# Kernel optimization log

Hardware: AMD Instinct MI355X
Metric: run time of the kernel (lower is better)

## Reference

```python
import jax, jax.numpy as jnp
import numpy as np

B = 128          # episodes
L = 512          # static pad length per episode (support or query)
LAMBDA_K_TAU = 0.1


def _masked_cov(x, mask, lengths):
    # x: [B, L, D]; mask: [B, L, 1]; lengths: [B] (float counts)
    x = x * mask
    mean = x.sum(axis=1) / lengths[:, None]                    # [B, D]
    c = (x - mean[:, None, :]) * mask                          # [B, L, D]
    cov = jnp.einsum('bld,ble->bde', c, c)                     # [B, D, D]
    return cov / (lengths - 1.0)[:, None, None]


def _calc_label_cov_inv(task_cov, label_cov):
    d = task_cov.shape[-1]
    eye = jnp.eye(d, dtype=task_cov.dtype)
    m = LAMBDA_K_TAU * label_cov + (1.0 - LAMBDA_K_TAU) * task_cov + 0.1 * eye
    return jnp.linalg.inv(m)


def _separate_qsl(graph_reprs, labels, is_query, batch_index):
    # Re-batch flat [N, D] into padded per-episode support/query tensors.
    N, D = graph_reprs.shape
    g = batch_index * 2 + is_query                             # group id
    perm = jnp.argsort(g)                                      # stable sort
    gs = g[perm]
    first = jnp.searchsorted(gs, gs, side='left')
    rank = jnp.arange(N) - first                               # index within group
    b = batch_index[perm]
    q = is_query[perm]
    row_s = jnp.where(q == 0, rank, L)                         # dummy row L for other kind
    row_q = jnp.where(q == 1, rank, L)
    xp = graph_reprs[perm]
    sup = jnp.zeros((B, L + 1, D), graph_reprs.dtype).at[b, row_s].set(xp)[:, :L]
    qry = jnp.zeros((B, L + 1, D), graph_reprs.dtype).at[b, row_q].set(xp)[:, :L]
    sup_lab = jnp.zeros((B, L + 1), labels.dtype).at[b, row_s].set(labels[perm])[:, :L]
    isq = is_query.astype(jnp.float32)
    sup_len = jnp.zeros((B,), jnp.float32).at[batch_index].add(1.0 - isq)
    qry_len = jnp.zeros((B,), jnp.float32).at[batch_index].add(isq)
    return sup, sup_lab, sup_len, qry, qry_len


def setup_inputs() -> dict:
    key = jax.random.key(0)
    k0, k1, k2, k3 = jax.random.split(key, 4)
    N, D = 49152, 512
    graph_reprs = jax.random.normal(k0, (N, D), jnp.float32)
    labels = jax.random.randint(k1, (N,), 0, 2)
    is_query = jax.random.randint(k2, (N,), 0, 2)
    batch_index = jnp.sort(jax.random.randint(k3, (N,), 0, B))
    log_scale = jnp.full((1,), np.log(1.0 / 16.0), jnp.float32)
    return {"graph_reprs": graph_reprs, "log_scale": log_scale,
            "labels": labels, "is_query": is_query, "batch_index": batch_index}


def reference(graph_reprs, log_scale, labels, is_query, batch_index):
    sup, sup_lab, sup_len, qry, qry_len = _separate_qsl(graph_reprs, labels, is_query, batch_index)
    f = jnp.float32
    support_mask = (jnp.arange(L)[None, :] < sup_len[:, None]).astype(f)[..., None]  # [B,L,1]
    mpos = (sup_lab == 1).astype(f)[..., None] * support_mask
    mneg = (sup_lab == 0).astype(f)[..., None] * support_mask

    pos_mean = (sup * mpos).sum(axis=1) / mpos.sum(axis=1)     # [B, D]
    neg_mean = (sup * mneg).sum(axis=1) / mneg.sum(axis=1)

    task_cov = _masked_cov(sup, support_mask, sup_len)
    pos_cnt = mpos.sum(axis=(1, 2))
    neg_cnt = mneg.sum(axis=(1, 2))
    # Masked covariance == cov of boolean-extracted, re-batched class subsets.
    pos_cov = _masked_cov(sup, mpos, pos_cnt)
    neg_cov = _masked_cov(sup, mneg, neg_cnt)

    pos_inv = _calc_label_cov_inv(task_cov, pos_cov)
    neg_inv = _calc_label_cov_inv(task_cov, neg_cov)

    query_mask = (jnp.arange(L)[None, :] < qry_len[:, None]).astype(f)  # [B, L]
    pos_diff = qry - pos_mean[:, None, :]
    neg_diff = qry - neg_mean[:, None, :]
    # Faithful to original einsum (sums inv over its second index):
    pos_maha = jnp.einsum('bik,bkx,bij->bi', pos_diff, pos_inv, pos_diff) * query_mask
    neg_maha = jnp.einsum('bik,bkx,bij->bi', neg_diff, neg_inv, neg_diff) * query_mask

    logits = jnp.stack([neg_maha, pos_maha], axis=-1)          # [B, L, 2]
    return logits * jnp.exp(log_scale)
```

## Files before the change

kernel.cpp:

```cpp
#include <hip/hip_runtime.h>
#include <cstdint>
#include <cstddef>

#define EPISODES 128
#define LPAD     512
#define DDIM     512
#define NS_CAP   320
#define GTILE    64
#define NPAIRS   15
#define CG_ITERS 14
#define GL_F4    4096
#define KCH      64
#define XBF_ROW  1024
#define GREG     48

typedef __attribute__((ext_vector_type(8))) __bf16 bf16x8;
typedef __attribute__((ext_vector_type(4))) float  floatx4;

__device__ __forceinline__ int lower_bound_dev(const int* __restrict__ a, int n, int key){
    int lo = 0, hi = n;
    while(lo < hi){
        int m = (lo + hi) >> 1;
        if(a[m] < key) lo = m + 1; else hi = m;
    }
    return lo;
}

__device__ __forceinline__ float4 f4add(float4 a, float4 b){
    return make_float4(a.x+b.x, a.y+b.y, a.z+b.z, a.w+b.w);
}
__device__ __forceinline__ float4 f4fma(float s, float4 a, float4 acc){
    return make_float4(acc.x + s*a.x, acc.y + s*a.y, acc.z + s*a.z, acc.w + s*a.w);
}
__device__ __forceinline__ float f4dot(float4 a, float4 b){
    return a.x*b.x + a.y*b.y + a.z*b.z + a.w*b.w;
}
__device__ __forceinline__ float f4sum(float4 a){ return (a.x+a.y)+(a.z+a.w); }

__device__ __forceinline__ unsigned short f2bf(float x){
    unsigned u = __float_as_uint(x);
    u += 0x7FFFu + ((u >> 16) & 1u);
    return (unsigned short)(u >> 16);
}
__device__ __forceinline__ float bf2f(unsigned short h){
    return __uint_as_float(((unsigned)h) << 16);
}
__device__ __forceinline__ void cvt_hilo(float4 x, ushort4& hh, ushort4& ll){
    hh.x = f2bf(x.x); ll.x = f2bf(x.x - bf2f(hh.x));
    hh.y = f2bf(x.y); ll.y = f2bf(x.y - bf2f(hh.y));
    hh.z = f2bf(x.z); ll.z = f2bf(x.z - bf2f(hh.z));
    hh.w = f2bf(x.w); ll.w = f2bf(x.w - bf2f(hh.w));
}

__device__ __forceinline__ float rdlanef(float v, int l){
    return __int_as_float(__builtin_amdgcn_readlane(__float_as_int(v), l));
}
__device__ __forceinline__ float dotb(float4 g, float4 u, int l){
    return g.x*rdlanef(u.x,l) + g.y*rdlanef(u.y,l)
         + g.z*rdlanef(u.z,l) + g.w*rdlanef(u.w,l);
}
__device__ __forceinline__ void gload_lds16(const void* g, void* l){
    __builtin_amdgcn_global_load_lds(
        (const __attribute__((address_space(1))) void*)g,
        (__attribute__((address_space(3))) void*)l,
        16, 0, 0);
}

__global__ __launch_bounds__(256) void k_prep(
        const int* __restrict__ labels, const int* __restrict__ is_query,
        const int* __restrict__ bidx, const float* __restrict__ X, int N,
        int* __restrict__ sup_idx, int* __restrict__ qry_idx,
        int* __restrict__ sup_lab, int* __restrict__ counts,
        float* __restrict__ task_mean, float* __restrict__ pos_mean,
        float* __restrict__ neg_mean, float* __restrict__ row_sums2,
        unsigned short* __restrict__ Xbf)
{
    const int bid  = blockIdx.x;
    const int b    = bid >> 1;
    const int h    = bid & 1;
    const int tid  = threadIdx.x;
    const int lane = tid & 63;
    const int wave = tid >> 6;

    __shared__ int s_start, s_end;
    __shared__ int wq[4];
    __shared__ int s_runq, s_npos;
    __shared__ int   sidx[NS_CAP];
    __shared__ float slabf[NS_CAP];
    __shared__ float4 pa[4][64];
    __shared__ float4 pp[4][64];

    if(tid == 0){
        s_start = lower_bound_dev(bidx, N, b);
        s_end   = lower_bound_dev(bidx, N, b + 1);
        s_runq  = 0;
        s_npos  = 0;
    }
    __syncthreads();
    const int start = s_start, end = s_end;

    for(int base = start; base < end; base += 256){
        int idx   = base + tid;
        bool valid = idx < end;
        int q   = valid ? is_query[idx] : 0;
        int lab = valid ? labels[idx]   : 0;
        unsigned long long m = __ballot(q == 1);
        if(lane == 0) wq[wave] = __popcll(m);
        __syncthreads();
        int woff = 0;
        for(int w = 0; w < wave; w++) woff += wq[w];
        int qbefore = __popcll(m & ((1ull << lane) - 1ull)) + woff;
        int runq0 = s_runq;
        int chunk_total = wq[0] + wq[1] + wq[2] + wq[3];
        if(valid){
            int pos_in_seg = idx - start;
            if(q){
                int qr = runq0 + qbefore;
                if(h == 0 && qr < LPAD) qry_idx[b * LPAD + qr] = idx;
            } else {
                int sr = pos_in_seg - runq0 - qbefore;
                if(sr < LPAD){
                    if(h == 0){
                        sup_idx[b * LPAD + sr] = idx;
                        sup_lab[b * LPAD + sr] = lab;
                    }
                    if(sr < NS_CAP){ sidx[sr] = idx; slabf[sr] = (float)lab; }
                    if(lab == 1) atomicAdd(&s_npos, 1);
                }
            }
        }
        __syncthreads();
        if(tid == 0) s_runq = runq0 + chunk_total;
        __syncthreads();
    }

    const int nq   = s_runq;
    const int ns   = (end - start) - nq;
    const int npos = s_npos;
    const int nneg = ns - npos;
    if(h == 0 && tid == 0){
        counts[b*4 + 0] = ns;
        counts[b*4 + 1] = nq;
        counts[b*4 + 2] = npos;
        counts[b*4 + 3] = nneg;
    }
    const int nsb = min(ns, NS_CAP);

    const float4* X4 = (const float4*)X;
    const int colg = h*64 + lane;
    float4 sa = make_float4(0.f,0.f,0.f,0.f);
    float4 sp = make_float4(0.f,0.f,0.f,0.f);
    int r = wave;
    for(; r + 12 < nsb; r += 16){
        int n0 = sidx[r], n1 = sidx[r+4], n2 = sidx[r+8], n3 = sidx[r+12];
        float l0 = slabf[r], l1 = slabf[r+4], l2 = slabf[r+8], l3 = slabf[r+12];
        float4 x0 = X4[(size_t)n0*128 + colg];
        float4 x1 = X4[(size_t)n1*128 + colg];
        float4 x2 = X4[(size_t)n2*128 + colg];
        float4 x3 = X4[(size_t)n3*128 + colg];
        sa = f4add(sa, f4add(f4add(x0,x1), f4add(x2,x3)));
        sp = f4fma(l0,x0, f4fma(l1,x1, f4fma(l2,x2, f4fma(l3,x3, sp))));
        {
            ushort4 hh, ll;
            size_t rb;
            rb = ((size_t)(b*NS_CAP + r   ) << 10);
            cvt_hilo(x0, hh, ll);
            *(ushort4*)&Xbf[rb + colg*4] = hh;  *(ushort4*)&Xbf[rb + 512 + colg*4] = ll;
            rb = ((size_t)(b*NS_CAP + r+4 ) << 10);
            cvt_hilo(x1, hh, ll);
            *(ushort4*)&Xbf[rb + colg*4] = hh;  *(ushort4*)&Xbf[rb + 512 + colg*4] = ll;
            rb = ((size_t)(b*NS_CAP + r+8 ) << 10);
            cvt_hilo(x2, hh, ll);
            *(ushort4*)&Xbf[rb + colg*4] = hh;  *(ushort4*)&Xbf[rb + 512 + colg*4] = ll;
            rb = ((size_t)(b*NS_CAP + r+12) << 10);
            cvt_hilo(x3, hh, ll);
            *(ushort4*)&Xbf[rb + colg*4] = hh;  *(ushort4*)&Xbf[rb + 512 + colg*4] = ll;
        }
        float r0s = f4sum(x0), r1s = f4sum(x1), r2s = f4sum(x2), r3s = f4sum(x3);
        #pragma unroll
        for(int off = 32; off; off >>= 1){
            r0s += __shfl_xor(r0s, off); r1s += __shfl_xor(r1s, off);
            r2s += __shfl_xor(r2s, off); r3s += __shfl_xor(r3s, off);
        }
        if(lane == 0){
            row_sums2[(b*LPAD + r   )*2 + h] = r0s;
            row_sums2[(b*LPAD + r+4 )*2 + h] = r1s;
            row_sums2[(b*LPAD + r+8 )*2 + h] = r2s;
            row_sums2[(b*LPAD + r+12)*2 + h] = r3s;
        }
    }
    for(; r < nsb; r += 4){
        int n = sidx[r];
        float l = slabf[r];
        float4 x = X4[(size_t)n*128 + colg];
        sa = f4add(sa, x);
        sp = f4fma(l, x, sp);
        {
            ushort4 hh, ll;
            size_t rb = ((size_t)(b*NS_CAP + r) << 10);
            cvt_hilo(x, hh, ll);
            *(ushort4*)&Xbf[rb + colg*4] = hh;  *(ushort4*)&Xbf[rb + 512 + colg*4] = ll;
        }
        float rs = f4sum(x);
        #pragma unroll
        for(int off = 32; off; off >>= 1) rs += __shfl_xor(rs, off);
        if(lane == 0) row_sums2[(b*LPAD + r)*2 + h] = rs;
    }
    {
        const int padf = min((nsb + 63) & ~63, NS_CAP);
        ushort4 z; z.x = z.y = z.z = z.w = 0;
        for(int rz = nsb + wave; rz < padf; rz += 4){
            size_t rb = ((size_t)(b*NS_CAP + rz) << 10);
            *(ushort4*)&Xbf[rb + colg*4] = z;
            *(ushort4*)&Xbf[rb + 512 + colg*4] = z;
        }
    }
    pa[wave][lane] = sa;
    pp[wave][lane] = sp;
    __syncthreads();
    if(tid < 64){
        float4 A = f4add(f4add(pa[0][tid],pa[1][tid]), f4add(pa[2][tid],pa[3][tid]));
        float4 P = f4add(f4add(pp[0][tid],pp[1][tid]), f4add(pp[2][tid],pp[3][tid]));
        float4 Nn = make_float4(A.x-P.x, A.y-P.y, A.z-P.z, A.w-P.w);
        float ia = 1.f/(float)ns, ip = 1.f/(float)npos, in = 1.f/(float)nneg;
        int c = b*128 + h*64 + tid;
        ((float4*)task_mean)[c] = make_float4(A.x*ia, A.y*ia, A.z*ia, A.w*ia);
        ((float4*)pos_mean )[c] = make_float4(P.x*ip, P.y*ip, P.z*ip, P.w*ip);
        ((float4*)neg_mean )[c] = make_float4(Nn.x*in, Nn.y*in, Nn.z*in, Nn.w*in);
    }
}

__global__ __launch_bounds__(256) void k_gram(
        const unsigned short* __restrict__ Xbf,
        const int* __restrict__ counts, float* __restrict__ G0)
{
    const int bid = blockIdx.x;
    const int b   = bid / NPAIRS;
    int tp = bid % NPAIRS;
    int ti = 0;
    while((ti+1)*(ti+2)/2 <= tp) ti++;
    const int tj  = tp - ti*(ti+1)/2;
    const int tid = threadIdx.x;
    const int lane = tid & 63;
    const int wave = tid >> 6;

    const int ns  = counts[b*4 + 0];
    const int nsc = min(ns, NS_CAP);
    if(ti * GTILE >= nsc) return;
    const bool diag = (ti == tj);

    __shared__ __align__(16) unsigned short SM[4 * GTILE * 64];
    unsigned short* const SAh = SM;
    unsigned short* const SAl = SM + 4096;
    const unsigned short* Bh = diag ? SAh : (SM + 8192);
    const unsigned short* Bl = diag ? SAl : (SM + 12288);

    const int r8  = lane >> 3;
    const int blk = lane & 7;
    const int fr = lane & 15;
    const int fq = (lane >> 4) * 8;
    const int ry = (wave >> 1) * 32;
    const int cx = (wave & 1) * 32;

    floatx4 acc[2][2];
    acc[0][0] = (floatx4){0.f,0.f,0.f,0.f};
    acc[0][1] = (floatx4){0.f,0.f,0.f,0.f};
    acc[1][0] = (floatx4){0.f,0.f,0.f,0.f};
    acc[1][1] = (floatx4){0.f,0.f,0.f,0.f};

    const int xr = blk ^ r8;
    for(int k0 = 0; k0 < DDIM; k0 += KCH){
        __syncthreads();
        #pragma unroll
        for(int i = 0; i < 4; i++){
            int e  = wave*4 + i;
            int pl = e >> 3, g = e & 7;
            int row = g*8 + r8;
            const unsigned short* src = Xbf
                + ((size_t)(b*NS_CAP + ti*GTILE + row) << 10)
                + pl*512 + k0 + (xr << 3);
            gload_lds16(src, SM + pl*4096 + row*64 + blk*8);
        }
        if(!diag){
            #pragma unroll
            for(int i = 0; i < 4; i++){
                int e  = wave*4 + i;
                int pl = e >> 3, g = e & 7;
                int row = g*8 + r8;
                const unsigned short* src = Xbf
                    + ((size_t)(b*NS_CAP + tj*GTILE + row) << 10)
                    + pl*512 + k0 + (xr << 3);
                gload_lds16(src, SM + 8192 + pl*4096 + row*64 + blk*8);
            }
        }
        __syncthreads();
        #pragma unroll
        for(int ks = 0; ks < KCH; ks += 32){
            const int j  = (ks + fq) >> 3;
            const int jx = (j ^ (fr & 7)) << 3;
            bf16x8 ah0 = *(const bf16x8*)&SAh[(ry      + fr)*64 + jx];
            bf16x8 ah1 = *(const bf16x8*)&SAh[(ry + 16 + fr)*64 + jx];
            bf16x8 al0 = *(const bf16x8*)&SAl[(ry      + fr)*64 + jx];
            bf16x8 al1 = *(const bf16x8*)&SAl[(ry + 16 + fr)*64 + jx];
            bf16x8 bh0 = *(const bf16x8*)&Bh [(cx      + fr)*64 + jx];
            bf16x8 bh1 = *(const bf16x8*)&Bh [(cx + 16 + fr)*64 + jx];
            bf16x8 bl0 = *(const bf16x8*)&Bl [(cx      + fr)*64 + jx];
            bf16x8 bl1 = *(const bf16x8*)&Bl [(cx + 16 + fr)*64 + jx];
            acc[0][0] = __builtin_amdgcn_mfma_f32_16x16x32_bf16(ah0, bh0, acc[0][0], 0,0,0);
            acc[0][1] = __builtin_amdgcn_mfma_f32_16x16x32_bf16(ah0, bh1, acc[0][1], 0,0,0);
            acc[1][0] = __builtin_amdgcn_mfma_f32_16x16x32_bf16(ah1, bh0, acc[1][0], 0,0,0);
            acc[1][1] = __builtin_amdgcn_mfma_f32_16x16x32_bf16(ah1, bh1, acc[1][1], 0,0,0);
            acc[0][0] = __builtin_amdgcn_mfma_f32_16x16x32_bf16(ah0, bl0, acc[0][0], 0,0,0);
            acc[0][1] = __builtin_amdgcn_mfma_f32_16x16x32_bf16(ah0, bl1, acc[0][1], 0,0,0);
            acc[1][0] = __builtin_amdgcn_mfma_f32_16x16x32_bf16(ah1, bl0, acc[1][0], 0,0,0);
            acc[1][1] = __builtin_amdgcn_mfma_f32_16x16x32_bf16(ah1, bl1, acc[1][1], 0,0,0);
            acc[0][0] = __builtin_amdgcn_mfma_f32_16x16x32_bf16(al0, bh0, acc[0][0], 0,0,0);
            acc[0][1] = __builtin_amdgcn_mfma_f32_16x16x32_bf16(al0, bh1, acc[0][1], 0,0,0);
            acc[1][0] = __builtin_amdgcn_mfma_f32_16x16x32_bf16(al1, bh0, acc[1][0], 0,0,0);
            acc[1][1] = __builtin_amdgcn_mfma_f32_16x16x32_bf16(al1, bh1, acc[1][1], 0,0,0);
        }
    }

    float4* Gf4 = (float4*)(G0 + (size_t)b * NS_CAP * NS_CAP);
    const int q = lane >> 4, j = lane & 15;
    #pragma unroll
    for(int sy = 0; sy < 2; sy++)
        #pragma unroll
        for(int sx = 0; sx < 2; sx++){
            int cq = ((ti*GTILE + ry + sy*16) >> 2) + q;
            int t  = tj*GTILE + cx + sx*16 + j;
            Gf4[(size_t)cq * NS_CAP + t] =
                make_float4(acc[sy][sx].x, acc[sy][sx].y, acc[sy][sx].z, acc[sy][sx].w);
        }

    if(!diag){
        __syncthreads();
        float* Tb = (float*)SM;
        #pragma unroll
        for(int sy = 0; sy < 2; sy++)
            #pragma unroll
            for(int sx = 0; sx < 2; sx++){
                int r0 = ry + sy*16 + 4*q;
                int c  = cx + sx*16 + j;
                Tb[(r0+0)*68 + c] = acc[sy][sx].x;
                Tb[(r0+1)*68 + c] = acc[sy][sx].y;
                Tb[(r0+2)*68 + c] = acc[sy][sx].z;
                Tb[(r0+3)*68 + c] = acc[sy][sx].w;
            }
        __syncthreads();
        for(int e = tid; e < 16*GTILE; e += 256){
            int cc = e >> 6;
            int r  = e & 63;
            float4 v = *(const float4*)&Tb[r*68 + 4*cc];
            Gf4[(size_t)(tj*16 + cc) * NS_CAP + ti*GTILE + r] = v;
        }
    }
}

extern __shared__ float4 gl4[];

__global__ __launch_bounds__(512) void k_cgc(
        const float* __restrict__ X, const float* __restrict__ G0,
        const int* __restrict__ sup_idx, const int* __restrict__ sup_lab,
        const int* __restrict__ counts, const float* __restrict__ row_sums2,
        float* __restrict__ vout)
{
    const int bid  = blockIdx.x;
    const int sys  = ((bid & 7) << 5) | (bid >> 3);
    const int b    = sys >> 1;
    const int cls  = sys & 1;
    const int tid  = threadIdx.x;
    const int lane = tid & 63;
    const int wave = tid >> 6;

    __shared__ __align__(16) float u[NS_CAP];
    __shared__ int   idx_l[NS_CAP];
    __shared__ float P[64];

    const int ns   = counts[b*4 + 0];
    const int nsc  = min(ns, NS_CAP);
    const int ncls = cls ? counts[b*4 + 2] : counts[b*4 + 3];
    const float c_task = 0.9f / (float)(ns - 1);
    const float c_cls  = 0.1f / (float)(ncls - 1);
    const float inv_ns = 1.f / (float)ns;
    const float inv_nc = 1.f / (float)ncls;
    const float4* G4 = (const float4*)(G0 + (size_t)b * NS_CAP * NS_CAP);
    const float4* u4 = (const float4*)u;
    const int nf4 = (nsc + 3) >> 2;

    const bool mth = tid < NS_CAP;
    const bool own = tid < nsc;
    float mfl = 0.f, sraw = 0.f;
    if(own){
        mfl  = (sup_lab[b*LPAD + tid] == cls) ? 1.f : 0.f;
        float2 rs = ((const float2*)row_sums2)[b*LPAD + tid];
        sraw = rs.x + rs.y;
    }
    for(int s = tid; s < nsc; s += 512) idx_l[s] = sup_idx[b*LPAD + s];
    if(tid < 64) P[tid] = 0.f;

    const bool fastu   = (nf4 <= 64);
    const bool haverow = ((wave << 6) < nsc);

    float4 g[GREG];
    if(fastu && haverow){
        #pragma unroll
        for(int c4 = 0; c4 < GREG; c4++){
            float4 v = G4[(size_t)c4 * NS_CAP + tid];
            bool live = (4*c4 < nsc);
            g[c4].x = live ? v.x : 0.f;
            g[c4].y = live ? v.y : 0.f;
            g[c4].z = live ? v.z : 0.f;
            g[c4].w = live ? v.w : 0.f;
        }
    }

    if(fastu && nf4 > GREG){
        const int nchunk = (nsc + 63) >> 6;
        for(int ch = 0; ch < nchunk; ch++){
            const int t = (ch << 6) + lane;
            const bool act = t < nsc;
            for(int c4 = GREG + wave; c4 < nf4; c4 += 8){
                if(act) gload_lds16(G4 + (size_t)c4 * NS_CAP + t,
                                    gl4 + (c4 - GREG) * nsc + t);
            }
        }
    }
    __syncthreads();

    auto bundle = [&](float v0, float v1, float v2, float v3, float v4,
                      float* S){
        #pragma unroll
        for(int off = 32; off; off >>= 1){
            v0 += __shfl_xor(v0, off); v1 += __shfl_xor(v1, off);
            v2 += __shfl_xor(v2, off); v3 += __shfl_xor(v3, off);
            v4 += __shfl_xor(v4, off);
        }
        if(lane == 0){
            P[wave*8 + 0] = v0; P[wave*8 + 1] = v1; P[wave*8 + 2] = v2;
            P[wave*8 + 3] = v3; P[wave*8 + 4] = v4;
        }
        __syncthreads();
        float pv = P[lane];
        pv += __shfl_xor(pv, 8);
        pv += __shfl_xor(pv, 16);
        pv += __shfl_xor(pv, 32);
        S[0] = __shfl(pv, 0); S[1] = __shfl(pv, 1); S[2] = __shfl(pv, 2);
        S[3] = __shfl(pv, 3); S[4] = __shfl(pv, 4);
    };

    auto matvec = [&]() -> float {
        float t = 0.f;
        if(fastu){
            if(haverow){
                float4 ubc = u4[lane < nf4 ? lane : 0];
                asm volatile("" : "+v"(ubc.x), "+v"(ubc.y), "+v"(ubc.z), "+v"(ubc.w));
                float s0 = 0.f, s1 = 0.f, s2 = 0.f, s3 = 0.f;
                #pragma unroll
                for(int c4 = 0; c4 < GREG; c4 += 4){
                    s0 += dotb(g[c4+0], ubc, c4+0);
                    s1 += dotb(g[c4+1], ubc, c4+1);
                    s2 += dotb(g[c4+2], ubc, c4+2);
                    s3 += dotb(g[c4+3], ubc, c4+3);
                }
                if(nf4 > GREG){
                    const int row = own ? tid : (nsc - 1);
                    for(int c4 = GREG; c4 < nf4; c4++)
                        s0 += f4dot(gl4[(c4 - GREG)*nsc + row], u4[c4]);
                }
                t = (s0 + s1) + (s2 + s3);
            }
            return own ? t : 0.f;
        } else {
            float s0 = 0.f, s1 = 0.f, s2 = 0.f, s3 = 0.f;
            if(own){
                int c4 = 0;
                for(; c4 + 4 <= nf4; c4 += 4){
                    float4 h0 = G4[(size_t)(c4+0)*NS_CAP + tid];
                    float4 h1 = G4[(size_t)(c4+1)*NS_CAP + tid];
                    float4 h2 = G4[(size_t)(c4+2)*NS_CAP + tid];
                    float4 h3 = G4[(size_t)(c4+3)*NS_CAP + tid];
                    s0 += f4dot(h0, u4[c4+0]); s1 += f4dot(h1, u4[c4+1]);
                    s2 += f4dot(h2, u4[c4+2]); s3 += f4dot(h3, u4[c4+3]);
                }
                for(; c4 < nf4; c4++) s0 += f4dot(G4[(size_t)c4*NS_CAP + tid], u4[c4]);
            }
            float tt = (s0 + s1) + (s2 + s3);
            return own ? tt : 0.f;
        }
    };

    float S[5];
    bundle(sraw, mfl * sraw, 0.f, 0.f, 0.f, S);
    float A0 = S[0] * inv_ns, A1 = S[1] * inv_nc;
    float cr = own ? -10.f * (c_task*(sraw - A0) + mfl*c_cls*(sraw - A1)) : 0.f;
    if(mth) u[tid] = cr;
    __syncthreads();
    float tr = matvec();

    float cp = 0.f, cq = 0.f, tq = 0.f, cx = 0.f;
    float gamma_old = 1.f, alpha_old = 1.f;
    bool first = true;

    for(int it = 0; it < CG_ITERS; ++it){
        bundle(tr, mfl*tr, tr*tr, mfl*tr*tr, tr*cr, S);
        A0 = S[0] * inv_ns; A1 = S[1] * inv_nc;
        float gamma = S[4];
        float delta = 0.1f*gamma + c_task*(S[2] - S[0]*A0)
                                 + c_cls *(S[3] - S[1]*A1);
        float beta  = first ? 0.f : gamma / gamma_old;
        float denom = first ? delta : (delta - beta * gamma / alpha_old);
        float alpha = (gamma < 1e-30f) ? 0.f : gamma / denom;
        float ur = own ? (c_task*(tr - A0) + mfl*c_cls*(tr - A1)) : 0.f;
        float cw = 0.1f*cr + ur;
        cp = cr + beta * cp;
        cq = cw + beta * cq;
        cx += alpha * cp;
        if(it == CG_ITERS - 1 || gamma < 1e-26f) break;
        if(mth) u[tid] = ur;
        __syncthreads();
        float gv = matvec();
        float tw = 0.1f*tr + gv;
        tq = tw + beta * tq;
        cr -= alpha * cq;
        tr -= alpha * tq;
        gamma_old = gamma; alpha_old = alpha; first = false;
    }

    __syncthreads();
    if(mth) u[tid] = own ? cx : 0.f;
    __syncthreads();
    const float4* X4 = (const float4*)X;
    const int f4c = tid & 127;
    const int rg  = tid >> 7;
    float4 acc = make_float4(0.f,0.f,0.f,0.f);
    int s = rg;
    for(; s + 28 < nsc; s += 32){
        int n0 = idx_l[s],    n1 = idx_l[s+4],  n2 = idx_l[s+8],  n3 = idx_l[s+12];
        int n4 = idx_l[s+16], n5 = idx_l[s+20], n6 = idx_l[s+24], n7 = idx_l[s+28];
        float w0 = u[s],    w1 = u[s+4],  w2 = u[s+8],  w3 = u[s+12];
        float w4 = u[s+16], w5 = u[s+20], w6 = u[s+24], w7 = u[s+28];
        float4 x0 = X4[(size_t)n0*128 + f4c];
        float4 x1 = X4[(size_t)n1*128 + f4c];
        float4 x2 = X4[(size_t)n2*128 + f4c];
        float4 x3 = X4[(size_t)n3*128 + f4c];
        float4 x4 = X4[(size_t)n4*128 + f4c];
        float4 x5 = X4[(size_t)n5*128 + f4c];
        float4 x6 = X4[(size_t)n6*128 + f4c];
        float4 x7 = X4[(size_t)n7*128 + f4c];
        acc = f4fma(w0,x0, f4fma(w1,x1, f4fma(w2,x2, f4fma(w3,x3, acc))));
        acc = f4fma(w4,x4, f4fma(w5,x5, f4fma(w6,x6, f4fma(w7,x7, acc))));
    }
    for(; s < nsc; s += 4)
        acc = f4fma(u[s], X4[(size_t)idx_l[s]*128 + f4c], acc);
    gl4[rg*128 + f4c] = acc;
    __syncthreads();
    if(tid < 128){
        float4 v = f4add(f4add(gl4[tid], gl4[128+tid]),
                         f4add(gl4[256+tid], gl4[384+tid]));
        v.x += 10.f; v.y += 10.f; v.z += 10.f; v.w += 10.f;
        ((float4*)vout)[(size_t)sys * 128 + tid] = v;
    }
}

__global__ __launch_bounds__(256) void k_out(
        const float* __restrict__ X,
        const int* __restrict__ qry_idx, const int* __restrict__ counts,
        const float* __restrict__ pos_mean, const float* __restrict__ neg_mean,
        const float* __restrict__ vsol, const float* __restrict__ log_scale,
        float* __restrict__ out)
{
    const int bid  = blockIdx.x;
    const int b    = bid >> 1;
    const int h    = bid & 1;
    const int tid  = threadIdx.x;
    const int lane = tid & 63;
    const int wave = tid >> 6;

    __shared__ __align__(16) float vpos[DDIM];
    __shared__ __align__(16) float vneg[DDIM];
    __shared__ float red4[4][4];
    __shared__ float sc[4];

    const int nq  = counts[b*4 + 1];
    const int nqc = min(nq, LPAD);
    const float scale = expf(log_scale[0]);

    float pm0 = pos_mean[b*DDIM + tid], pm1 = pos_mean[b*DDIM + tid + 256];
    float nm0 = neg_mean[b*DDIM + tid], nm1 = neg_mean[b*DDIM + tid + 256];
    float vp0 = vsol[(size_t)(b*2 + 1) * DDIM + tid];
    float vp1 = vsol[(size_t)(b*2 + 1) * DDIM + tid + 256];
    float vn0 = vsol[(size_t)(b*2 + 0) * DDIM + tid];
    float vn1 = vsol[(size_t)(b*2 + 0) * DDIM + tid + 256];
    vpos[tid] = vp0; vpos[tid + 256] = vp1;
    vneg[tid] = vn0; vneg[tid + 256] = vn1;

    float smp = pm0 + pm1;
    float smn = nm0 + nm1;
    float mvp = pm0 * vp0 + pm1 * vp1;
    float mvn = nm0 * vn0 + nm1 * vn1;
    #pragma unroll
    for(int off = 32; off; off >>= 1){
        smp += __shfl_xor(smp, off);
        smn += __shfl_xor(smn, off);
        mvp += __shfl_xor(mvp, off);
        mvn += __shfl_xor(mvn, off);
    }
    if(lane == 0){
        red4[wave][0] = smp; red4[wave][1] = smn;
        red4[wave][2] = mvp; red4[wave][3] = mvn;
    }
    __syncthreads();
    if(tid < 4) sc[tid] = red4[0][tid] + red4[1][tid] + red4[2][tid] + red4[3][tid];
    __syncthreads();

    const float4* vp4 = (const float4*)vpos;
    const float4* vn4 = (const float4*)vneg;
    const float4 vpa = vp4[lane], vpb = vp4[lane + 64];
    const float4 vna = vn4[lane], vnb = vn4[lane + 64];
    for(int r = wave + 4*h; r < nqc; r += 16){
        int r2 = r + 8;
        bool has2 = r2 < nqc;
        int n  = qry_idx[b * LPAD + r];
        int n2 = qry_idx[b * LPAD + (has2 ? r2 : r)];
        const float4* xr = (const float4*)(X + (size_t)n  * DDIM);
        const float4* yr = (const float4*)(X + (size_t)n2 * DDIM);
        float4 x0 = xr[lane], x1 = xr[lane + 64];
        float4 y0 = yr[lane], y1 = yr[lane + 64];
        float tp = f4dot(x0, vpa) + f4dot(x1, vpb);
        float tn = f4dot(x0, vna) + f4dot(x1, vnb);
        float sx = f4sum(x0) + f4sum(x1);
        float tp2 = f4dot(y0, vpa) + f4dot(y1, vpb);
        float tn2 = f4dot(y0, vna) + f4dot(y1, vnb);
        float sx2 = f4sum(y0) + f4sum(y1);
        #pragma unroll
        for(int off = 32; off; off >>= 1){
            tp  += __shfl_xor(tp,  off);
            tn  += __shfl_xor(tn,  off);
            sx  += __shfl_xor(sx,  off);
            tp2 += __shfl_xor(tp2, off);
            tn2 += __shfl_xor(tn2, off);
            sx2 += __shfl_xor(sx2, off);
        }
        if(lane == 0){
            float mp = (tp - sc[2]) * (sx - sc[0]);
            float mn = (tn - sc[3]) * (sx - sc[1]);
            ((float2*)out)[(size_t)b * LPAD + r] = make_float2(mn * scale, mp * scale);
            if(has2){
                float mp2 = (tp2 - sc[2]) * (sx2 - sc[0]);
                float mn2 = (tn2 - sc[3]) * (sx2 - sc[1]);
                ((float2*)out)[(size_t)b * LPAD + r2] = make_float2(mn2 * scale, mp2 * scale);
            }
        }
    }
    const int lo = max(nqc, h * 256), hi = (h + 1) * 256;
    for(int r = lo + tid; r < hi; r += 256)
        ((float2*)out)[(size_t)b * LPAD + r] = make_float2(0.f, 0.f);
}

extern "C" void kernel_launch(void* const* d_in, const int* in_sizes, int n_in,
                              void* d_out, int out_size, void* d_ws, size_t ws_size,
                              hipStream_t stream)
{
    const float* X         = (const float*)d_in[0];
    const float* log_scale = (const float*)d_in[1];
    const int*   labels    = (const int*)d_in[2];
    const int*   is_query  = (const int*)d_in[3];
    const int*   bidx      = (const int*)d_in[4];
    const int N = in_sizes[2];

    char* ws = (char*)d_ws;
    auto alloc = [&](size_t bytes) -> char* {
        char* p = ws;
        ws += (bytes + 255) & ~(size_t)255;
        return p;
    };
    int*   sup_idx   = (int*)  alloc((size_t)EPISODES * LPAD * sizeof(int));
    int*   qry_idx   = (int*)  alloc((size_t)EPISODES * LPAD * sizeof(int));
    int*   sup_lab   = (int*)  alloc((size_t)EPISODES * LPAD * sizeof(int));
    int*   counts    = (int*)  alloc((size_t)EPISODES * 4 * sizeof(int));
    float* task_mean = (float*)alloc((size_t)EPISODES * DDIM * sizeof(float));
    float* pos_mean  = (float*)alloc((size_t)EPISODES * DDIM * sizeof(float));
    float* neg_mean  = (float*)alloc((size_t)EPISODES * DDIM * sizeof(float));
    float* vsol      = (float*)alloc((size_t)EPISODES * 2 * DDIM * sizeof(float));
    float* row_sums2 = (float*)alloc((size_t)EPISODES * LPAD * 2 * sizeof(float));
    float* G0        = (float*)alloc((size_t)EPISODES * NS_CAP * NS_CAP * sizeof(float));
    unsigned short* Xbf = (unsigned short*)alloc(
                          (size_t)EPISODES * NS_CAP * XBF_ROW * sizeof(unsigned short));
    (void)ws_size;
    (void)task_mean;

    k_prep<<<EPISODES*2, 256, 0, stream>>>(labels, is_query, bidx, X, N,
                                           sup_idx, qry_idx, sup_lab, counts,
                                           task_mean, pos_mean, neg_mean, row_sums2,
                                           Xbf);
    k_gram<<<EPISODES * NPAIRS, 256, 0, stream>>>(Xbf, counts, G0);
    k_cgc<<<EPISODES * 2, 512, GL_F4 * sizeof(float4), stream>>>(
                                            X, G0, sup_idx, sup_lab, counts,
                                            row_sums2, vsol);
    k_out<<<EPISODES*2, 256, 0, stream>>>(X, qry_idx, counts, pos_mean, neg_mean,
                                          vsol, log_scale, (float*)d_out);
}
```

Before: 287.9 us.

## Fuse query Mahalanobis output stage into the CG solve kernel

Removes the separate k_out kernel. Each k_cgc block now scores all query rows for its own class right after solving for v, keeping v in shared memory instead of writing vsol to global memory. This saves a launch and the vsol round trip. In exchange, each query row of X is read twice, once per class block, and each output element is written as a separate scalar rather than a float2 pair.

```diff
diff --git a/kernel.cpp b/kernel.cpp
--- a/kernel.cpp
+++ b/kernel.cpp
@@ -363,7 +363,9 @@
         const float* __restrict__ X, const float* __restrict__ G0,
         const int* __restrict__ sup_idx, const int* __restrict__ sup_lab,
         const int* __restrict__ counts, const float* __restrict__ row_sums2,
-        float* __restrict__ vout)
+        const int* __restrict__ qry_idx,
+        const float* __restrict__ pos_mean, const float* __restrict__ neg_mean,
+        const float* __restrict__ log_scale, float* __restrict__ out)
 {
     const int bid  = blockIdx.x;
     const int sys  = ((bid & 7) << 5) | (bid >> 3);
@@ -375,10 +377,14 @@
 
     __shared__ __align__(16) float u[NS_CAP];
     __shared__ int   idx_l[NS_CAP];
+    __shared__ int   qidx_l[LPAD];
     __shared__ float P[64];
+    __shared__ __align__(16) float4 vv[128];
 
     const int ns   = counts[b*4 + 0];
     const int nsc  = min(ns, NS_CAP);
+    const int nq   = counts[b*4 + 1];
+    const int nqc  = min(nq, LPAD);
     const int ncls = cls ? counts[b*4 + 2] : counts[b*4 + 3];
     const float c_task = 0.9f / (float)(ns - 1);
     const float c_cls  = 0.1f / (float)(ncls - 1);
@@ -397,6 +403,7 @@
         sraw = rs.x + rs.y;
     }
     for(int s = tid; s < nsc; s += 512) idx_l[s] = sup_idx[b*LPAD + s];
+    qidx_l[tid] = qry_idx[b*LPAD + tid];
     if(tid < 64) P[tid] = 0.f;
 
     const bool fastu   = (nf4 <= 64);
@@ -559,103 +566,50 @@
         float4 v = f4add(f4add(gl4[tid], gl4[128+tid]),
                          f4add(gl4[256+tid], gl4[384+tid]));
         v.x += 10.f; v.y += 10.f; v.z += 10.f; v.w += 10.f;
-        ((float4*)vout)[(size_t)sys * 128 + tid] = v;
-    }
-}
-
-__global__ __launch_bounds__(256) void k_out(
-        const float* __restrict__ X,
-        const int* __restrict__ qry_idx, const int* __restrict__ counts,
-        const float* __restrict__ pos_mean, const float* __restrict__ neg_mean,
-        const float* __restrict__ vsol, const float* __restrict__ log_scale,
-        float* __restrict__ out)
-{
-    const int bid  = blockIdx.x;
-    const int b    = bid >> 1;
-    const int h    = bid & 1;
-    const int tid  = threadIdx.x;
-    const int lane = tid & 63;
-    const int wave = tid >> 6;
-
-    __shared__ __align__(16) float vpos[DDIM];
-    __shared__ __align__(16) float vneg[DDIM];
-    __shared__ float red4[4][4];
-    __shared__ float sc[4];
-
-    const int nq  = counts[b*4 + 1];
-    const int nqc = min(nq, LPAD);
+        vv[tid] = v;
+    }
+
+    const float* mean_c = cls ? pos_mean : neg_mean;
+    float psm = 0.f, pmv = 0.f;
+    if(tid < 128){
+        float4 m4 = ((const float4*)mean_c)[b*128 + tid];
+        float4 v  = vv[tid];
+        psm = f4sum(m4);
+        pmv = f4dot(m4, v);
+    }
+    bundle(psm, pmv, 0.f, 0.f, 0.f, S);
+    const float sm = S[0], mv = S[1];
     const float scale = expf(log_scale[0]);
 
-    float pm0 = pos_mean[b*DDIM + tid], pm1 = pos_mean[b*DDIM + tid + 256];
-    float nm0 = neg_mean[b*DDIM + tid], nm1 = neg_mean[b*DDIM + tid + 256];
-    float vp0 = vsol[(size_t)(b*2 + 1) * DDIM + tid];
-    float vp1 = vsol[(size_t)(b*2 + 1) * DDIM + tid + 256];
-    float vn0 = vsol[(size_t)(b*2 + 0) * DDIM + tid];
-    float vn1 = vsol[(size_t)(b*2 + 0) * DDIM + tid + 256];
-    vpos[tid] = vp0; vpos[tid + 256] = vp1;
-    vneg[tid] = vn0; vneg[tid + 256] = vn1;
-
-    float smp = pm0 + pm1;
-    float smn = nm0 + nm1;
-    float mvp = pm0 * vp0 + pm1 * vp1;
-    float mvn = nm0 * vn0 + nm1 * vn1;
-    #pragma unroll
-    for(int off = 32; off; off >>= 1){
-        smp += __shfl_xor(smp, off);
-        smn += __shfl_xor(smn, off);
-        mvp += __shfl_xor(mvp, off);
-        mvn += __shfl_xor(mvn, off);
-    }
-    if(lane == 0){
-        red4[wave][0] = smp; red4[wave][1] = smn;
-        red4[wave][2] = mvp; red4[wave][3] = mvn;
-    }
-    __syncthreads();
-    if(tid < 4) sc[tid] = red4[0][tid] + red4[1][tid] + red4[2][tid] + red4[3][tid];
-    __syncthreads();
-
-    const float4* vp4 = (const float4*)vpos;
-    const float4* vn4 = (const float4*)vneg;
-    const float4 vpa = vp4[lane], vpb = vp4[lane + 64];
-    const float4 vna = vn4[lane], vnb = vn4[lane + 64];
-    for(int r = wave + 4*h; r < nqc; r += 16){
+    const float4 va = vv[lane], vb = vv[lane + 64];
+    for(int r = wave; r < nqc; r += 16){
         int r2 = r + 8;
         bool has2 = r2 < nqc;
-        int n  = qry_idx[b * LPAD + r];
-        int n2 = qry_idx[b * LPAD + (has2 ? r2 : r)];
+        int n  = qidx_l[r];
+        int n2 = qidx_l[has2 ? r2 : r];
         const float4* xr = (const float4*)(X + (size_t)n  * DDIM);
         const float4* yr = (const float4*)(X + (size_t)n2 * DDIM);
         float4 x0 = xr[lane], x1 = xr[lane + 64];
         float4 y0 = yr[lane], y1 = yr[lane + 64];
-        float tp = f4dot(x0, vpa) + f4dot(x1, vpb);
-        float tn = f4dot(x0, vna) + f4dot(x1, vnb);
-        float sx = f4sum(x0) + f4sum(x1);
-        float tp2 = f4dot(y0, vpa) + f4dot(y1, vpb);
-        float tn2 = f4dot(y0, vna) + f4dot(y1, vnb);
-        float sx2 = f4sum(y0) + f4sum(y1);
+        float t1 = f4dot(x0, va) + f4dot(x1, vb);
+        float s1 = f4sum(x0) + f4sum(x1);
+        float t2 = f4dot(y0, va) + f4dot(y1, vb);
+        float s2 = f4sum(y0) + f4sum(y1);
         #pragma unroll
         for(int off = 32; off; off >>= 1){
-            tp  += __shfl_xor(tp,  off);
-            tn  += __shfl_xor(tn,  off);
-            sx  += __shfl_xor(sx,  off);
-            tp2 += __shfl_xor(tp2, off);
-            tn2 += __shfl_xor(tn2, off);
-            sx2 += __shfl_xor(sx2, off);
+            t1 += __shfl_xor(t1, off);
+            s1 += __shfl_xor(s1, off);
+            t2 += __shfl_xor(t2, off);
+            s2 += __shfl_xor(s2, off);
         }
         if(lane == 0){
-            float mp = (tp - sc[2]) * (sx - sc[0]);
-            float mn = (tn - sc[3]) * (sx - sc[1]);
-            ((float2*)out)[(size_t)b * LPAD + r] = make_float2(mn * scale, mp * scale);
-            if(has2){
-                float mp2 = (tp2 - sc[2]) * (sx2 - sc[0]);
-                float mn2 = (tn2 - sc[3]) * (sx2 - sc[1]);
-                ((float2*)out)[(size_t)b * LPAD + r2] = make_float2(mn2 * scale, mp2 * scale);
-            }
-        }
-    }
-    const int lo = max(nqc, h * 256), hi = (h + 1) * 256;
-    for(int r = lo + tid; r < hi; r += 256)
-        ((float2*)out)[(size_t)b * LPAD + r] = make_float2(0.f, 0.f);
+            out[(size_t)(b*LPAD + r)*2 + cls] = (t1 - mv) * (s1 - sm) * scale;
+            if(has2)
+                out[(size_t)(b*LPAD + r2)*2 + cls] = (t2 - mv) * (s2 - sm) * scale;
+        }
+    }
+    for(int r = nqc + tid; r < LPAD; r += 512)
+        out[(size_t)(b*LPAD + r)*2 + cls] = 0.f;
 }
 
 extern "C" void kernel_launch(void* const* d_in, const int* in_sizes, int n_in,
@@ -682,7 +636,6 @@
     float* task_mean = (float*)alloc((size_t)EPISODES * DDIM * sizeof(float));
     float* pos_mean  = (float*)alloc((size_t)EPISODES * DDIM * sizeof(float));
     float* neg_mean  = (float*)alloc((size_t)EPISODES * DDIM * sizeof(float));
-    float* vsol      = (float*)alloc((size_t)EPISODES * 2 * DDIM * sizeof(float));
     float* row_sums2 = (float*)alloc((size_t)EPISODES * LPAD * 2 * sizeof(float));
     float* G0        = (float*)alloc((size_t)EPISODES * NS_CAP * NS_CAP * sizeof(float));
     unsigned short* Xbf = (unsigned short*)alloc(
@@ -697,7 +650,6 @@
     k_gram<<<EPISODES * NPAIRS, 256, 0, stream>>>(Xbf, counts, G0);
     k_cgc<<<EPISODES * 2, 512, GL_F4 * sizeof(float4), stream>>>(
                                             X, G0, sup_idx, sup_lab, counts,
-                                            row_sums2, vsol);
-    k_out<<<EPISODES*2, 256, 0, stream>>>(X, qry_idx, counts, pos_mean, neg_mean,
-                                          vsol, log_scale, (float*)d_out);
-}
+                                            row_sums2, qry_idx, pos_mean, neg_mean,
+                                            log_scale, (float*)d_out);
+}
```

Measured after the change: 273.3 us. -5.0%, faster.
